# Optimization experiments

Hardware: AMD Instinct MI355X
Metric: run time of the kernel (lower is better)

## Reference

```python
import jax, jax.numpy as jnp
import numpy as np

B, DIN, DOUT = 8192, 4096, 4096
BIAS_OFFSET = 512.0


def setup_inputs() -> dict:
    key = jax.random.key(0)
    kx, kw = jax.random.split(key)
    x = jax.random.normal(kx, (B, DIN), dtype=jnp.float32)
    # Ternary weights in {-1, 0, 1}, iid with zero_prob=0.5 and mean 0:
    # P(0)=0.5, P(-1)=P(1)=0.25
    u = jax.random.uniform(kw, (DIN, DOUT))
    W = jnp.where(u < 0.25, -1.0, jnp.where(u < 0.5, 1.0, 0.0)).astype(jnp.float32)
    b = jnp.full((DOUT,), BIAS_OFFSET, dtype=jnp.float32)
    return {"x": x, "W": W, "b": b}


def reference(x, W, b):
    # z: pre-activation of ternary-weight linear layer  [B, DOUT]
    z = jnp.matmul(x, W) + b
    # binarized activation (sign with ties -> +1), as in TernBin forward
    x_out = jnp.where(z >= 0, 1.0, -1.0).astype(z.dtype)
    return (x_out, z)
```

## Files before the change

### kernel.cpp

```cpp
#include <hip/hip_runtime.h>
#include <stdint.h>

#define MDIM 8192
#define NDIM 4096
#define KDIM 4096

#define BM 256
#define BN 256
#define BK 64
#define NT (KDIM / BK)

#define CVT_X_BLOCKS 16384
#define CVT_W_BLOCKS 4096

typedef __bf16 bf16x8 __attribute__((ext_vector_type(8)));
typedef float f32x4 __attribute__((ext_vector_type(4)));

#define GPTR(p) ((const __attribute__((address_space(1))) void*)(p))
#define LPTR(p) ((__attribute__((address_space(3))) void*)(p))

#define BAR() asm volatile("s_barrier" ::: "memory")

__device__ __forceinline__ uint32_t f2bf(float f) {
  union { float f; uint32_t u; } c; c.f = f;
  uint32_t u = c.u;
  u += 0x7fffu + ((u >> 16) & 1u);
  return u >> 16;
}

__global__ __launch_bounds__(256) void cvt_fused(const float* __restrict__ x,
                                                 const float* __restrict__ W,
                                                 unsigned short* __restrict__ xb,
                                                 unsigned short* __restrict__ Wt) {
  __shared__ uint32_t T[64][37];
  const int bid = blockIdx.x;
  const int t = threadIdx.x;
  if (bid < CVT_X_BLOCKS) {
    size_t i = ((size_t)bid * 256 + t) * 8;
    const float4* p = (const float4*)(x + i);
    float4 a = p[0], b = p[1];
    uint4 r;
    r.x = f2bf(a.x) | (f2bf(a.y) << 16);
    r.y = f2bf(a.z) | (f2bf(a.w) << 16);
    r.z = f2bf(b.x) | (f2bf(b.y) << 16);
    r.w = f2bf(b.z) | (f2bf(b.w) << 16);
    *(uint4*)(xb + i) = r;
  } else {
    const int wb = bid - CVT_X_BLOCKS;
    const int n0 = (wb & 63) * 64;
    const int k0 = (wb >> 6) * 64;
    const int nl = t & 63;
    const int kpb = t >> 6;
#pragma unroll
    for (int i = 0; i < 8; ++i) {
      int kp = kpb + 4 * i;
      int k = 2 * kp;
      float v0 = W[(size_t)(k0 + k) * NDIM + n0 + nl];
      float v1 = W[(size_t)(k0 + k + 1) * NDIM + n0 + nl];
      T[nl][kp] = f2bf(v0) | (f2bf(v1) << 16);
    }
    __syncthreads();
    const int ch = t & 7;
    const int nb = t >> 3;
#pragma unroll
    for (int h = 0; h < 2; ++h) {
      int n = nb + 32 * h;
      uint4 v;
      v.x = T[n][ch * 4 + 0];
      v.y = T[n][ch * 4 + 1];
      v.z = T[n][ch * 4 + 2];
      v.w = T[n][ch * 4 + 3];
      *(uint4*)&Wt[(size_t)(n0 + n) * KDIM + k0 + ch * 8] = v;
    }
  }
}


__device__ __forceinline__ void stage2(unsigned short* dst,
                                       const unsigned short* G, int half,
                                       int tile, int wave) {
#pragma unroll
  for (int i = 0; i < 2; ++i) {
    const int rb = half * 128 + i * 64;
    __builtin_amdgcn_global_load_lds(
        GPTR(G + (size_t)rb * KDIM + (size_t)tile * 64),
        LPTR(dst + (rb + wave * 8) * BK), 16, 0, 0);
  }
}

template <int IB>
__device__ __forceinline__ void load_a4k(const unsigned short* buf, int wm,
                                         int rA, int koff, bf16x8 (&a)[4]) {
#pragma unroll
  for (int i = 0; i < 4; ++i)
    a[i] = *(const bf16x8*)(buf + (size_t)(wm * 128 + (IB + i) * 16 + rA) * BK +
                            koff);
}

__device__ __forceinline__ void load_b4k(const unsigned short* buf, int wn,
                                         int rA, int koff, bf16x8 (&b)[4]) {
#pragma unroll
  for (int j = 0; j < 4; ++j)
    b[j] = *(const bf16x8*)(buf + (size_t)(wn * 64 + j * 16 + rA) * BK + koff);
}

template <int IB>
__device__ __forceinline__ void mfma16q(const bf16x8 (&a)[4],
                                        const bf16x8 (&b)[4],
                                        f32x4 (&acc)[8][4]) {
  __builtin_amdgcn_s_setprio(1);
#pragma unroll
  for (int i = 0; i < 4; ++i)
#pragma unroll
    for (int j = 0; j < 4; ++j)
      acc[IB + i][j] = __builtin_amdgcn_mfma_f32_16x16x32_bf16(
          b[j], a[i], acc[IB + i][j], 0, 0, 0);
  __builtin_amdgcn_s_setprio(0);
}

template <bool SA, bool SB, int VM>
__device__ __forceinline__ void tile_step(
    const unsigned short* curA, unsigned short* curB, unsigned short* nxtA,
    int T, const unsigned short* Ag, const unsigned short* Bg, int wave,
    int wm, int wn, int rA, int k0off, int k1off, f32x4 (&acc)[8][4]) {
  bf16x8 aL[4], aH[4], b0[4], b1[4];
  load_a4k<0>(curA, wm, rA, k0off, aL);
  load_b4k(curB, wn, rA, k0off, b0);
  if (SA) stage2(nxtA, Ag, 0, T + 1, wave);
  BAR();
  mfma16q<0>(aL, b0, acc);
  BAR();
  load_a4k<0>(curA, wm, rA, k1off, aH);
  load_b4k(curB, wn, rA, k1off, b1);
  if (SA) stage2(nxtA, Ag, 1, T + 1, wave);
  BAR();
  mfma16q<0>(aH, b1, acc);
  BAR();
  load_a4k<4>(curA, wm, rA, k0off, aL);
  load_a4k<4>(curA, wm, rA, k1off, aH);
  if (SB) stage2(curB, Bg, 0, T + 2, wave);
  BAR();
  mfma16q<4>(aL, b0, acc);
  BAR();
  if (SB) stage2(curB, Bg, 1, T + 2, wave);
  if constexpr (VM == 4) asm volatile("s_waitcnt vmcnt(4)" ::: "memory");
  else if constexpr (VM == 0) asm volatile("s_waitcnt vmcnt(0)" ::: "memory");
  BAR();
  mfma16q<4>(aH, b1, acc);
  BAR();
}

__global__ __launch_bounds__(512, 2) void gemm_bf16_8ph(
    const unsigned short* __restrict__ Ab, const unsigned short* __restrict__ Bt,
    const float* __restrict__ bias, float* __restrict__ out) {
  __shared__ __align__(16) unsigned short lds[4 * BM * BK];
  unsigned short* A0 = lds;
  unsigned short* B0 = lds + 1 * BM * BK;
  unsigned short* A1 = lds + 2 * BM * BK;
  unsigned short* B1 = lds + 3 * BM * BK;

  const int tid = threadIdx.x;
  const int lane = tid & 63;
  const int wave = tid >> 6;
  const int wm = wave & 1;
  const int wn = wave >> 1;

  const int bid = blockIdx.x;
  const int wg = (bid & 7) * 64 + (bid >> 3);
  const int m0 = (wg >> 4) * BM;
  const int n0 = (wg & 15) * BN;

  f32x4 acc[8][4];
#pragma unroll
  for (int i = 0; i < 8; ++i)
#pragma unroll
    for (int j = 0; j < 4; ++j) {
      f32x4 z = {0.0f, 0.0f, 0.0f, 0.0f};
      acc[i][j] = z;
    }

  const int tr = tid >> 3;
  const int tc = (tid & 7) ^ (tr & 7);
  const unsigned short* Ag = Ab + (size_t)(m0 + tr) * KDIM + tc * 8;
  const unsigned short* Bg = Bt + (size_t)(n0 + tr) * KDIM + tc * 8;

  const int rA = lane & 15;
  const int hi = lane >> 4;
  const int key = lane & 7;
  const int k0off = ((0 + hi) ^ key) * 8;
  const int k1off = ((4 + hi) ^ key) * 8;

  stage2(B0, Bg, 0, 0, wave);
  stage2(B0, Bg, 1, 0, wave);
  stage2(A0, Ag, 0, 0, wave);
  stage2(A0, Ag, 1, 0, wave);
  stage2(B1, Bg, 0, 1, wave);
  stage2(B1, Bg, 1, 1, wave);
  asm volatile("s_waitcnt vmcnt(4)" ::: "memory");
  BAR();

  for (int T = 0; T < NT - 2; T += 2) {
    tile_step<true, true, 4>(A0, B0, A1, T, Ag, Bg, wave, wm, wn, rA, k0off,
                             k1off, acc);
    tile_step<true, true, 4>(A1, B1, A0, T + 1, Ag, Bg, wave, wm, wn, rA,
                             k0off, k1off, acc);
  }
  tile_step<true, false, 0>(A0, B0, A1, NT - 2, Ag, Bg, wave, wm, wn, rA,
                            k0off, k1off, acc);
  tile_step<false, false, -1>(A1, B1, A0, NT - 1, Ag, Bg, wave, wm, wn, rA,
                              k0off, k1off, acc);

  float* zout = out + (size_t)MDIM * NDIM;
  const int ml = lane & 15;
  const int nb4 = (lane >> 4) * 4;
#pragma unroll
  for (int i = 0; i < 8; ++i) {
    int m = m0 + wm * 128 + i * 16 + ml;
    float* zrow = zout + (size_t)m * NDIM;
    float* srow = out + (size_t)m * NDIM;
#pragma unroll
    for (int j = 0; j < 4; ++j) {
      int n = n0 + wn * 64 + j * 16 + nb4;
      float4 bv = *(const float4*)&bias[n];
      f32x4 v = acc[i][j];
      float4 z, s;
      z.x = v[0] + bv.x; z.y = v[1] + bv.y; z.z = v[2] + bv.z; z.w = v[3] + bv.w;
      s.x = (z.x >= 0.0f) ? 1.0f : -1.0f;
      s.y = (z.y >= 0.0f) ? 1.0f : -1.0f;
      s.z = (z.z >= 0.0f) ? 1.0f : -1.0f;
      s.w = (z.w >= 0.0f) ? 1.0f : -1.0f;
      *(float4*)&zrow[n] = z;
      *(float4*)&srow[n] = s;
    }
  }
}

__device__ __forceinline__ void mfma_step128(const unsigned short* As,
                                             const unsigned short* Bs,
                                             f32x4 acc[4][4], int lane, int wm,
                                             int wn) {
  const int rA = lane & 15;
  const int key = lane & 7;
#pragma unroll
  for (int kk = 0; kk < 2; ++kk) {
    const int koff = ((kk * 4 + (lane >> 4)) ^ key) * 8;
    bf16x8 a[4], b[4];
#pragma unroll
    for (int i = 0; i < 4; ++i) {
      a[i] = *(const bf16x8*)(As + (size_t)(wm * 64 + i * 16 + rA) * 64 + koff);
      b[i] = *(const bf16x8*)(Bs + (size_t)(wn * 64 + i * 16 + rA) * 64 + koff);
    }
#pragma unroll
    for (int i = 0; i < 4; ++i)
#pragma unroll
      for (int j = 0; j < 4; ++j)
        acc[i][j] = __builtin_amdgcn_mfma_f32_16x16x32_bf16(b[j], a[i],
                                                            acc[i][j], 0, 0, 0);
  }
}

__global__ __launch_bounds__(256) void gemm_bf16_nows(
    const float* __restrict__ x, const float* __restrict__ W,
    const float* __restrict__ bias, float* __restrict__ out) {
  __shared__ __align__(16) unsigned short As[128 * 64];
  __shared__ __align__(16) unsigned short Bs[128 * 64];

  const int tid = threadIdx.x;
  const int lane = tid & 63;
  const int wave = tid >> 6;
  const int wm = wave & 1;
  const int wn = wave >> 1;
  const int m0 = blockIdx.y * 128;
  const int n0 = blockIdx.x * 128;

  f32x4 acc[4][4];
#pragma unroll
  for (int i = 0; i < 4; ++i)
#pragma unroll
    for (int j = 0; j < 4; ++j) {
      f32x4 z = {0.0f, 0.0f, 0.0f, 0.0f};
      acc[i][j] = z;
    }

  for (int k0 = 0; k0 < KDIM; k0 += 64) {
    {
      const int kc = (tid & 15) * 4;
      const int cb = kc >> 3;
      const int wi = kc & 7;
      const int rowb = tid >> 4;
#pragma unroll
      for (int r = 0; r < 8; ++r) {
        int row = rowb + 16 * r;
        float4 v = *(const float4*)&x[(size_t)(m0 + row) * KDIM + k0 + kc];
        uint2 pk;
        pk.x = f2bf(v.x) | (f2bf(v.y) << 16);
        pk.y = f2bf(v.z) | (f2bf(v.w) << 16);
        *(uint2*)&As[row * 64 + ((cb ^ (row & 7)) * 8) + wi] = pk;
      }
    }
    {
      const int nc = (tid & 31) * 4;
      const int kb = tid >> 5;
#pragma unroll
      for (int r = 0; r < 8; ++r) {
        int krow = kb + 8 * r;
        int cb = krow >> 3, wi = krow & 7;
        float4 v = *(const float4*)&W[(size_t)(k0 + krow) * NDIM + n0 + nc];
        Bs[(nc + 0) * 64 + ((cb ^ ((nc + 0) & 7)) * 8) + wi] = (unsigned short)f2bf(v.x);
        Bs[(nc + 1) * 64 + ((cb ^ ((nc + 1) & 7)) * 8) + wi] = (unsigned short)f2bf(v.y);
        Bs[(nc + 2) * 64 + ((cb ^ ((nc + 2) & 7)) * 8) + wi] = (unsigned short)f2bf(v.z);
        Bs[(nc + 3) * 64 + ((cb ^ ((nc + 3) & 7)) * 8) + wi] = (unsigned short)f2bf(v.w);
      }
    }
    __syncthreads();
    mfma_step128(As, Bs, acc, lane, wm, wn);
    __syncthreads();
  }

  float* zout = out + (size_t)MDIM * NDIM;
  const int ml = lane & 15;
  const int nb4 = (lane >> 4) * 4;
#pragma unroll
  for (int i = 0; i < 4; ++i) {
    int m = m0 + wm * 64 + i * 16 + ml;
    float* zrow = zout + (size_t)m * NDIM;
    float* srow = out + (size_t)m * NDIM;
#pragma unroll
    for (int j = 0; j < 4; ++j) {
      int n = n0 + wn * 64 + j * 16 + nb4;
      float4 bv = *(const float4*)&bias[n];
      f32x4 v = acc[i][j];
      float4 z, s;
      z.x = v[0] + bv.x; z.y = v[1] + bv.y; z.z = v[2] + bv.z; z.w = v[3] + bv.w;
      s.x = (z.x >= 0.0f) ? 1.0f : -1.0f;
      s.y = (z.y >= 0.0f) ? 1.0f : -1.0f;
      s.z = (z.z >= 0.0f) ? 1.0f : -1.0f;
      s.w = (z.w >= 0.0f) ? 1.0f : -1.0f;
      *(float4*)&zrow[n] = z;
      *(float4*)&srow[n] = s;
    }
  }
}

extern "C" void kernel_launch(void* const* d_in, const int* in_sizes, int n_in,
                              void* d_out, int out_size, void* d_ws,
                              size_t ws_size, hipStream_t stream) {
  (void)in_sizes; (void)n_in; (void)out_size;
  const float* x = (const float*)d_in[0];
  const float* W = (const float*)d_in[1];
  const float* b = (const float*)d_in[2];
  float* out = (float*)d_out;

  const size_t xb_elems = (size_t)MDIM * KDIM;
  const size_t wt_elems = (size_t)KDIM * NDIM;
  const size_t need = (xb_elems + wt_elems) * sizeof(unsigned short);

  if (ws_size >= need) {
    unsigned short* xb = (unsigned short*)d_ws;
    unsigned short* wt = xb + xb_elems;
    cvt_fused<<<CVT_X_BLOCKS + CVT_W_BLOCKS, 256, 0, stream>>>(x, W, xb, wt);
    gemm_bf16_8ph<<<(MDIM / BM) * (NDIM / BN), 512, 0, stream>>>(xb, wt, b, out);
  } else {
    dim3 fgrid(NDIM / 128, MDIM / 128);
    gemm_bf16_nows<<<fgrid, 256, 0, stream>>>(x, W, b, out);
  }
}
```

Measured before the change: 601.6 us.

## Switch main GEMM from 16x16x32 to 32x32x16 bf16 MFMA tiles

Replaces the 16x16x32 MFMA instructions with 32x32x16 bf16 MFMA in the main 256x256 GEMM kernel. Each wave now holds 4x2 32x32 accumulator blocks, with new LDS fragment loads and swizzle offsets and a rewritten epilogue for the 32x32 output layout. The larger instruction tile reuses each LDS fragment across more output, which cuts LDS reads per FLOP. In exchange, the per-phase schedule between loads, barriers and MFMAs changes, and the LDS bank-access pattern under the existing swizzle may differ.

```diff
diff --git a/kernel.cpp b/kernel.cpp
--- a/kernel.cpp
+++ b/kernel.cpp
@@ -15,6 +15,7 @@
 
 typedef __bf16 bf16x8 __attribute__((ext_vector_type(8)));
 typedef float f32x4 __attribute__((ext_vector_type(4)));
+typedef float f32x16 __attribute__((ext_vector_type(16)));
 
 #define GPTR(p) ((const __attribute__((address_space(1))) void*)(p))
 #define LPTR(p) ((__attribute__((address_space(3))) void*)(p))
@@ -88,33 +89,39 @@
   }
 }
 
-template <int IB>
-__device__ __forceinline__ void load_a4k(const unsigned short* buf, int wm,
-                                         int rA, int koff, bf16x8 (&a)[4]) {
-#pragma unroll
-  for (int i = 0; i < 4; ++i)
-    a[i] = *(const bf16x8*)(buf + (size_t)(wm * 128 + (IB + i) * 16 + rA) * BK +
-                            koff);
-}
-
-__device__ __forceinline__ void load_b4k(const unsigned short* buf, int wn,
-                                         int rA, int koff, bf16x8 (&b)[4]) {
-#pragma unroll
-  for (int j = 0; j < 4; ++j)
-    b[j] = *(const bf16x8*)(buf + (size_t)(wn * 64 + j * 16 + rA) * BK + koff);
-}
-
-template <int IB>
-__device__ __forceinline__ void mfma16q(const bf16x8 (&a)[4],
-                                        const bf16x8 (&b)[4],
-                                        f32x4 (&acc)[8][4]) {
+template <int MH>
+__device__ __forceinline__ void load_a(const unsigned short* buf, int wm,
+                                       int r32, const int (&koff)[4],
+                                       bf16x8 (&a)[2][4]) {
+#pragma unroll
+  for (int i = 0; i < 2; ++i) {
+    const unsigned short* p =
+        buf + (size_t)(wm * 128 + (MH * 2 + i) * 32 + r32) * BK;
+#pragma unroll
+    for (int s = 0; s < 4; ++s) a[i][s] = *(const bf16x8*)(p + koff[s]);
+  }
+}
+
+template <int J>
+__device__ __forceinline__ void load_b(const unsigned short* buf, int wn,
+                                       int r32, const int (&koff)[4],
+                                       bf16x8 (&b)[4]) {
+  const unsigned short* p = buf + (size_t)(wn * 64 + J * 32 + r32) * BK;
+#pragma unroll
+  for (int s = 0; s < 4; ++s) b[s] = *(const bf16x8*)(p + koff[s]);
+}
+
+template <int IB, int J>
+__device__ __forceinline__ void mfma8(const bf16x8 (&a)[2][4],
+                                      const bf16x8 (&b)[4],
+                                      f32x16 (&acc)[4][2]) {
   __builtin_amdgcn_s_setprio(1);
 #pragma unroll
-  for (int i = 0; i < 4; ++i)
-#pragma unroll
-    for (int j = 0; j < 4; ++j)
-      acc[IB + i][j] = __builtin_amdgcn_mfma_f32_16x16x32_bf16(
-          b[j], a[i], acc[IB + i][j], 0, 0, 0);
+  for (int s = 0; s < 4; ++s)
+#pragma unroll
+    for (int i = 0; i < 2; ++i)
+      acc[IB + i][J] = __builtin_amdgcn_mfma_f32_32x32x16_bf16(
+          b[s], a[i][s], acc[IB + i][J], 0, 0, 0);
   __builtin_amdgcn_s_setprio(0);
 }
 
@@ -122,31 +129,29 @@
 __device__ __forceinline__ void tile_step(
     const unsigned short* curA, unsigned short* curB, unsigned short* nxtA,
     int T, const unsigned short* Ag, const unsigned short* Bg, int wave,
-    int wm, int wn, int rA, int k0off, int k1off, f32x4 (&acc)[8][4]) {
-  bf16x8 aL[4], aH[4], b0[4], b1[4];
-  load_a4k<0>(curA, wm, rA, k0off, aL);
-  load_b4k(curB, wn, rA, k0off, b0);
+    int wm, int wn, int r32, const int (&koff)[4], f32x16 (&acc)[4][2]) {
+  bf16x8 a[2][4], b0[4], b1[4];
+  load_a<0>(curA, wm, r32, koff, a);
+  load_b<0>(curB, wn, r32, koff, b0);
   if (SA) stage2(nxtA, Ag, 0, T + 1, wave);
   BAR();
-  mfma16q<0>(aL, b0, acc);
-  BAR();
-  load_a4k<0>(curA, wm, rA, k1off, aH);
-  load_b4k(curB, wn, rA, k1off, b1);
+  mfma8<0, 0>(a, b0, acc);
+  BAR();
+  load_b<1>(curB, wn, r32, koff, b1);
   if (SA) stage2(nxtA, Ag, 1, T + 1, wave);
   BAR();
-  mfma16q<0>(aH, b1, acc);
-  BAR();
-  load_a4k<4>(curA, wm, rA, k0off, aL);
-  load_a4k<4>(curA, wm, rA, k1off, aH);
+  mfma8<0, 1>(a, b1, acc);
+  BAR();
+  load_a<1>(curA, wm, r32, koff, a);
   if (SB) stage2(curB, Bg, 0, T + 2, wave);
   BAR();
-  mfma16q<4>(aL, b0, acc);
+  mfma8<2, 0>(a, b0, acc);
   BAR();
   if (SB) stage2(curB, Bg, 1, T + 2, wave);
   if constexpr (VM == 4) asm volatile("s_waitcnt vmcnt(4)" ::: "memory");
   else if constexpr (VM == 0) asm volatile("s_waitcnt vmcnt(0)" ::: "memory");
   BAR();
-  mfma16q<4>(aH, b1, acc);
+  mfma8<2, 1>(a, b1, acc);
   BAR();
 }
 
@@ -170,25 +175,25 @@
   const int m0 = (wg >> 4) * BM;
   const int n0 = (wg & 15) * BN;
 
-  f32x4 acc[8][4];
-#pragma unroll
-  for (int i = 0; i < 8; ++i)
-#pragma unroll
-    for (int j = 0; j < 4; ++j) {
-      f32x4 z = {0.0f, 0.0f, 0.0f, 0.0f};
-      acc[i][j] = z;
-    }
+  f32x16 acc[4][2];
+#pragma unroll
+  for (int i = 0; i < 4; ++i)
+#pragma unroll
+    for (int j = 0; j < 2; ++j)
+#pragma unroll
+      for (int e = 0; e < 16; ++e) acc[i][j][e] = 0.0f;
 
   const int tr = tid >> 3;
   const int tc = (tid & 7) ^ (tr & 7);
   const unsigned short* Ag = Ab + (size_t)(m0 + tr) * KDIM + tc * 8;
   const unsigned short* Bg = Bt + (size_t)(n0 + tr) * KDIM + tc * 8;
 
-  const int rA = lane & 15;
-  const int hi = lane >> 4;
+  const int r32 = lane & 31;
+  const int hi32 = lane >> 5;
   const int key = lane & 7;
-  const int k0off = ((0 + hi) ^ key) * 8;
-  const int k1off = ((4 + hi) ^ key) * 8;
+  int koff[4];
+#pragma unroll
+  for (int s = 0; s < 4; ++s) koff[s] = ((2 * s + hi32) ^ key) * 8;
 
   stage2(B0, Bg, 0, 0, wave);
   stage2(B0, Bg, 1, 0, wave);
@@ -200,22 +205,133 @@
   BAR();
 
   for (int T = 0; T < NT - 2; T += 2) {
-    tile_step<true, true, 4>(A0, B0, A1, T, Ag, Bg, wave, wm, wn, rA, k0off,
-                             k1off, acc);
-    tile_step<true, true, 4>(A1, B1, A0, T + 1, Ag, Bg, wave, wm, wn, rA,
-                             k0off, k1off, acc);
-  }
-  tile_step<true, false, 0>(A0, B0, A1, NT - 2, Ag, Bg, wave, wm, wn, rA,
-                            k0off, k1off, acc);
-  tile_step<false, false, -1>(A1, B1, A0, NT - 1, Ag, Bg, wave, wm, wn, rA,
-                              k0off, k1off, acc);
+    tile_step<true, true, 4>(A0, B0, A1, T, Ag, Bg, wave, wm, wn, r32, koff,
+                             acc);
+    tile_step<true, true, 4>(A1, B1, A0, T + 1, Ag, Bg, wave, wm, wn, r32,
+                             koff, acc);
+  }
+  tile_step<true, false, 0>(A0, B0, A1, NT - 2, Ag, Bg, wave, wm, wn, r32,
+                            koff, acc);
+  tile_step<false, false, -1>(A1, B1, A0, NT - 1, Ag, Bg, wave, wm, wn, r32,
+                              koff, acc);
+
+  float* zout = out + (size_t)MDIM * NDIM;
+  const int nq4 = 4 * hi32;
+#pragma unroll
+  for (int i = 0; i < 4; ++i) {
+    int m = m0 + wm * 128 + i * 32 + r32;
+    float* zrow = zout + (size_t)m * NDIM;
+    float* srow = out + (size_t)m * NDIM;
+#pragma unroll
+    for (int j = 0; j < 2; ++j) {
+#pragma unroll
+      for (int q = 0; q < 4; ++q) {
+        int n = n0 + wn * 64 + j * 32 + q * 8 + nq4;
+        float4 bv = *(const float4*)&bias[n];
+        float4 z, s;
+        z.x = acc[i][j][4 * q + 0] + bv.x;
+        z.y = acc[i][j][4 * q + 1] + bv.y;
+        z.z = acc[i][j][4 * q + 2] + bv.z;
+        z.w = acc[i][j][4 * q + 3] + bv.w;
+        s.x = (z.x >= 0.0f) ? 1.0f : -1.0f;
+        s.y = (z.y >= 0.0f) ? 1.0f : -1.0f;
+        s.z = (z.z >= 0.0f) ? 1.0f : -1.0f;
+        s.w = (z.w >= 0.0f) ? 1.0f : -1.0f;
+        *(float4*)&zrow[n] = z;
+        *(float4*)&srow[n] = s;
+      }
+    }
+  }
+}
+
+__device__ __forceinline__ void mfma_step128(const unsigned short* As,
+                                             const unsigned short* Bs,
+                                             f32x4 acc[4][4], int lane, int wm,
+                                             int wn) {
+  const int rA = lane & 15;
+  const int key = lane & 7;
+#pragma unroll
+  for (int kk = 0; kk < 2; ++kk) {
+    const int koff = ((kk * 4 + (lane >> 4)) ^ key) * 8;
+    bf16x8 a[4], b[4];
+#pragma unroll
+    for (int i = 0; i < 4; ++i) {
+      a[i] = *(const bf16x8*)(As + (size_t)(wm * 64 + i * 16 + rA) * 64 + koff);
+      b[i] = *(const bf16x8*)(Bs + (size_t)(wn * 64 + i * 16 + rA) * 64 + koff);
+    }
+#pragma unroll
+    for (int i = 0; i < 4; ++i)
+#pragma unroll
+      for (int j = 0; j < 4; ++j)
+        acc[i][j] = __builtin_amdgcn_mfma_f32_16x16x32_bf16(b[j], a[i],
+                                                            acc[i][j], 0, 0, 0);
+  }
+}
+
+__global__ __launch_bounds__(256) void gemm_bf16_nows(
+    const float* __restrict__ x, const float* __restrict__ W,
+    const float* __restrict__ bias, float* __restrict__ out) {
+  __shared__ __align__(16) unsigned short As[128 * 64];
+  __shared__ __align__(16) unsigned short Bs[128 * 64];
+
+  const int tid = threadIdx.x;
+  const int lane = tid & 63;
+  const int wave = tid >> 6;
+  const int wm = wave & 1;
+  const int wn = wave >> 1;
+  const int m0 = blockIdx.y * 128;
+  const int n0 = blockIdx.x * 128;
+
+  f32x4 acc[4][4];
+#pragma unroll
+  for (int i = 0; i < 4; ++i)
+#pragma unroll
+    for (int j = 0; j < 4; ++j) {
+      f32x4 z = {0.0f, 0.0f, 0.0f, 0.0f};
+      acc[i][j] = z;
+    }
+
+  for (int k0 = 0; k0 < KDIM; k0 += 64) {
+    {
+      const int kc = (tid & 15) * 4;
+      const int cb = kc >> 3;
+      const int wi = kc & 7;
+      const int rowb = tid >> 4;
+#pragma unroll
+      for (int r = 0; r < 8; ++r) {
+        int row = rowb + 16 * r;
+        float4 v = *(const float4*)&x[(size_t)(m0 + row) * KDIM + k0 + kc];
+        uint2 pk;
+        pk.x = f2bf(v.x) | (f2bf(v.y) << 16);
+        pk.y = f2bf(v.z) | (f2bf(v.w) << 16);
+        *(uint2*)&As[row * 64 + ((cb ^ (row & 7)) * 8) + wi] = pk;
+      }
+    }
+    {
+      const int nc = (tid & 31) * 4;
+      const int kb = tid >> 5;
+#pragma unroll
+      for (int r = 0; r < 8; ++r) {
+        int krow = kb + 8 * r;
+        int cb = krow >> 3, wi = krow & 7;
+        float4 v = *(const float4*)&W[(size_t)(k0 + krow) * NDIM + n0 + nc];
+        Bs[(nc + 0) * 64 + ((cb ^ ((nc + 0) & 7)) * 8) + wi] = (unsigned short)f2bf(v.x);
+        Bs[(nc + 1) * 64 + ((cb ^ ((nc + 1) & 7)) * 8) + wi] = (unsigned short)f2bf(v.y);
+        Bs[(nc + 2) * 64 + ((cb ^ ((nc + 2) & 7)) * 8) + wi] = (unsigned short)f2bf(v.z);
+        Bs[(nc + 3) * 64 + ((cb ^ ((nc + 3) & 7)) * 8) + wi] = (unsigned short)f2bf(v.w);
+      }
+    }
+    __syncthreads();
+    mfma_step128(As, Bs, acc, lane, wm, wn);
+    __syncthreads();
+  }
 
   float* zout = out + (size_t)MDIM * NDIM;
   const int ml = lane & 15;
   const int nb4 = (lane >> 4) * 4;
 #pragma unroll
-  for (int i = 0; i < 8; ++i) {
-    int m = m0 + wm * 128 + i * 16 + ml;
+  for (int i = 0; i < 4; ++i) {
+    int m = m0 + wm * 64 + i * 16 + ml;
     float* zrow = zout + (size_t)m * NDIM;
     float* srow = out + (size_t)m * NDIM;
 #pragma unroll
@@ -235,113 +351,6 @@
   }
 }
 
-__device__ __forceinline__ void mfma_step128(const unsigned short* As,
-                                             const unsigned short* Bs,
-                                             f32x4 acc[4][4], int lane, int wm,
-                                             int wn) {
-  const int rA = lane & 15;
-  const int key = lane & 7;
-#pragma unroll
-  for (int kk = 0; kk < 2; ++kk) {
-    const int koff = ((kk * 4 + (lane >> 4)) ^ key) * 8;
-    bf16x8 a[4], b[4];
-#pragma unroll
-    for (int i = 0; i < 4; ++i) {
-      a[i] = *(const bf16x8*)(As + (size_t)(wm * 64 + i * 16 + rA) * 64 + koff);
-      b[i] = *(const bf16x8*)(Bs + (size_t)(wn * 64 + i * 16 + rA) * 64 + koff);
-    }
-#pragma unroll
-    for (int i = 0; i < 4; ++i)
-#pragma unroll
-      for (int j = 0; j < 4; ++j)
-        acc[i][j] = __builtin_amdgcn_mfma_f32_16x16x32_bf16(b[j], a[i],
-                                                            acc[i][j], 0, 0, 0);
-  }
-}
-
-__global__ __launch_bounds__(256) void gemm_bf16_nows(
-    const float* __restrict__ x, const float* __restrict__ W,
-    const float* __restrict__ bias, float* __restrict__ out) {
-  __shared__ __align__(16) unsigned short As[128 * 64];
-  __shared__ __align__(16) unsigned short Bs[128 * 64];
-
-  const int tid = threadIdx.x;
-  const int lane = tid & 63;
-  const int wave = tid >> 6;
-  const int wm = wave & 1;
-  const int wn = wave >> 1;
-  const int m0 = blockIdx.y * 128;
-  const int n0 = blockIdx.x * 128;
-
-  f32x4 acc[4][4];
-#pragma unroll
-  for (int i = 0; i < 4; ++i)
-#pragma unroll
-    for (int j = 0; j < 4; ++j) {
-      f32x4 z = {0.0f, 0.0f, 0.0f, 0.0f};
-      acc[i][j] = z;
-    }
-
-  for (int k0 = 0; k0 < KDIM; k0 += 64) {
-    {
-      const int kc = (tid & 15) * 4;
-      const int cb = kc >> 3;
-      const int wi = kc & 7;
-      const int rowb = tid >> 4;
-#pragma unroll
-      for (int r = 0; r < 8; ++r) {
-        int row = rowb + 16 * r;
-        float4 v = *(const float4*)&x[(size_t)(m0 + row) * KDIM + k0 + kc];
-        uint2 pk;
-        pk.x = f2bf(v.x) | (f2bf(v.y) << 16);
-        pk.y = f2bf(v.z) | (f2bf(v.w) << 16);
-        *(uint2*)&As[row * 64 + ((cb ^ (row & 7)) * 8) + wi] = pk;
-      }
-    }
-    {
-      const int nc = (tid & 31) * 4;
-      const int kb = tid >> 5;
-#pragma unroll
-      for (int r = 0; r < 8; ++r) {
-        int krow = kb + 8 * r;
-        int cb = krow >> 3, wi = krow & 7;
-        float4 v = *(const float4*)&W[(size_t)(k0 + krow) * NDIM + n0 + nc];
-        Bs[(nc + 0) * 64 + ((cb ^ ((nc + 0) & 7)) * 8) + wi] = (unsigned short)f2bf(v.x);
-        Bs[(nc + 1) * 64 + ((cb ^ ((nc + 1) & 7)) * 8) + wi] = (unsigned short)f2bf(v.y);
-        Bs[(nc + 2) * 64 + ((cb ^ ((nc + 2) & 7)) * 8) + wi] = (unsigned short)f2bf(v.z);
-        Bs[(nc + 3) * 64 + ((cb ^ ((nc + 3) & 7)) * 8) + wi] = (unsigned short)f2bf(v.w);
-      }
-    }
-    __syncthreads();
-    mfma_step128(As, Bs, acc, lane, wm, wn);
-    __syncthreads();
-  }
-
-  float* zout = out + (size_t)MDIM * NDIM;
-  const int ml = lane & 15;
-  const int nb4 = (lane >> 4) * 4;
-#pragma unroll
-  for (int i = 0; i < 4; ++i) {
-    int m = m0 + wm * 64 + i * 16 + ml;
-    float* zrow = zout + (size_t)m * NDIM;
-    float* srow = out + (size_t)m * NDIM;
-#pragma unroll
-    for (int j = 0; j < 4; ++j) {
-      int n = n0 + wn * 64 + j * 16 + nb4;
-      float4 bv = *(const float4*)&bias[n];
-      f32x4 v = acc[i][j];
-      float4 z, s;
-      z.x = v[0] + bv.x; z.y = v[1] + bv.y; z.z = v[2] + bv.z; z.w = v[3] + bv.w;
-      s.x = (z.x >= 0.0f) ? 1.0f : -1.0f;
-      s.y = (z.y >= 0.0f) ? 1.0f : -1.0f;
-      s.z = (z.z >= 0.0f) ? 1.0f : -1.0f;
-      s.w = (z.w >= 0.0f) ? 1.0f : -1.0f;
-      *(float4*)&zrow[n] = z;
-      *(float4*)&srow[n] = s;
-    }
-  }
-}
-
 extern "C" void kernel_launch(void* const* d_in, const int* in_sizes, int n_in,
                               void* d_out, int out_size, void* d_ws,
                               size_t ws_size, hipStream_t stream) {
```

Measured after the change: 646.6 us. 7.5% more time.
